# Kernel tuning notes

Measured on AMD Instinct MI355X. Metric: run time of the kernel, lower is better.

The kernel has to match this reference:

```python
import jax, jax.numpy as jnp
import numpy as np

N_NODES = 50000
N_EDGES = 800000
N_GRAPHS = 64
F_IN, H1, H2, H3, N_CLS = 128, 512, 256, 128, 10
BN_EPS = 1e-5


def setup_inputs() -> dict:
    key = jax.random.key(0)
    ks = jax.random.split(key, 16)

    def lin(k, fi, fo):
        return jax.random.normal(k, (fi, fo), jnp.float32) / np.sqrt(fi).astype(np.float32)

    return {
        "x": jax.random.normal(ks[0], (N_NODES, F_IN), jnp.float32),
        "edge_index": jax.random.randint(ks[1], (2, N_EDGES), 0, N_NODES),
        "batch": jnp.sort(jax.random.randint(ks[2], (N_NODES,), 0, N_GRAPHS)),
        "W1": lin(ks[3], F_IN, H1), "b1": jnp.zeros((H1,), jnp.float32),
        "g1": jnp.ones((H1,), jnp.float32), "be1": jnp.zeros((H1,), jnp.float32),
        "W2": lin(ks[4], H1, H2), "b2": jnp.zeros((H2,), jnp.float32),
        "g2": jnp.ones((H2,), jnp.float32), "be2": jnp.zeros((H2,), jnp.float32),
        "W3": lin(ks[5], H2, H3), "b3": jnp.zeros((H3,), jnp.float32),
        "g3": jnp.ones((H3,), jnp.float32), "be3": jnp.zeros((H3,), jnp.float32),
        "Wo": lin(ks[6], H3, N_CLS), "bo": jnp.zeros((N_CLS,), jnp.float32),
    }


def _gcn_conv(x, row, col, W, b):
    # PyG GCNConv: h = x @ W; add self-loops; sym-normalized scatter-add; + bias
    n = x.shape[0]
    h = x @ W
    loop = jnp.arange(n, dtype=row.dtype)
    row2 = jnp.concatenate([row, loop])  # source nodes
    col2 = jnp.concatenate([col, loop])  # target nodes
    deg = jax.ops.segment_sum(jnp.ones_like(col2, dtype=h.dtype), col2, num_segments=n)
    dinv = jnp.where(deg > 0, jax.lax.rsqrt(deg), 0.0)
    norm = (dinv[row2] * dinv[col2])[:, None]
    agg = jax.ops.segment_sum(h[row2] * norm, col2, num_segments=n)
    return agg + b


def _bn(x, g, b):
    # training-mode BatchNorm over node dim (biased variance, eps=1e-5)
    mean = jnp.mean(x, axis=0)
    var = jnp.mean(jnp.square(x - mean), axis=0)
    return g * (x - mean) * jax.lax.rsqrt(var + BN_EPS) + b


def reference(x, edge_index, batch, W1, b1, g1, be1, W2, b2, g2, be2,
              W3, b3, g3, be3, Wo, bo):
    row, col = edge_index[0], edge_index[1]
    h = jax.nn.relu(_bn(_gcn_conv(x, row, col, W1, b1), g1, be1))
    h = jax.nn.relu(_bn(_gcn_conv(h, row, col, W2, b2), g2, be2))
    h = jax.nn.relu(_bn(_gcn_conv(h, row, col, W3, b3), g3, be3))
    # global_mean_pool over graph ids
    sums = jax.ops.segment_sum(h, batch, num_segments=N_GRAPHS)
    cnt = jax.ops.segment_sum(jnp.ones((h.shape[0],), h.dtype), batch, num_segments=N_GRAPHS)
    pooled = sums / jnp.maximum(cnt, 1.0)[:, None]
    return pooled @ Wo + bo
```

## Files before the change

### kernel.cpp

```cpp
#include <hip/hip_runtime.h>
#include <hip/hip_bf16.h>
#include <cstdint>
#include <cstddef>

#define NNODES 50000
#define NGRAPHS 64

typedef short bf16x8 __attribute__((ext_vector_type(8)));
typedef float f32x4 __attribute__((ext_vector_type(4)));

__device__ inline float bf2f(unsigned short u) {
    return __uint_as_float(((unsigned)u) << 16);
}
__device__ inline unsigned short f2bf(float f) {
    unsigned u = __float_as_uint(f);
    return (unsigned short)((u + 0x7fff + ((u >> 16) & 1)) >> 16);
}
__device__ inline void unpack8(uint4 u, float* v) {
    v[0] = bf2f((unsigned short)(u.x & 0xffff)); v[1] = bf2f((unsigned short)(u.x >> 16));
    v[2] = bf2f((unsigned short)(u.y & 0xffff)); v[3] = bf2f((unsigned short)(u.y >> 16));
    v[4] = bf2f((unsigned short)(u.z & 0xffff)); v[5] = bf2f((unsigned short)(u.z >> 16));
    v[6] = bf2f((unsigned short)(u.w & 0xffff)); v[7] = bf2f((unsigned short)(u.w >> 16));
}

__global__ void deg_count_k(const int* __restrict__ col, int* __restrict__ cnt, int ne) {
    int i = blockIdx.x * blockDim.x + threadIdx.x;
    if (i < ne) atomicAdd(&cnt[col[i]], 1);
}

__global__ __launch_bounds__(256) void scan1_k(const int* __restrict__ cnt, int* __restrict__ offs,
                                               int* __restrict__ bsum, float* __restrict__ dinv, int n) {
    int t = threadIdx.x;
    int base = blockIdx.x * 1024 + t * 4;
    int4 v = {0, 0, 0, 0};
    if (base + 3 < n) v = *reinterpret_cast<const int4*>(cnt + base);
    else {
        if (base + 0 < n) v.x = cnt[base + 0];
        if (base + 1 < n) v.y = cnt[base + 1];
        if (base + 2 < n) v.z = cnt[base + 2];
    }
    if (base + 0 < n) dinv[base + 0] = rsqrtf((float)(v.x + 1));
    if (base + 1 < n) dinv[base + 1] = rsqrtf((float)(v.y + 1));
    if (base + 2 < n) dinv[base + 2] = rsqrtf((float)(v.z + 1));
    if (base + 3 < n) dinv[base + 3] = rsqrtf((float)(v.w + 1));

    int s = v.x + v.y + v.z + v.w;
    __shared__ int lds[256];
    lds[t] = s;
    __syncthreads();
    #pragma unroll
    for (int d = 1; d < 256; d <<= 1) {
        int u = (t >= d) ? lds[t - d] : 0;
        __syncthreads();
        lds[t] += u;
        __syncthreads();
    }
    int excl = lds[t] - s;
    if (t == 255) bsum[blockIdx.x] = lds[t];

    if (base + 3 < n) {
        int4 o;
        o.x = excl; o.y = excl + v.x; o.z = o.y + v.y; o.w = o.z + v.z;
        *reinterpret_cast<int4*>(offs + base) = o;
    } else {
        int e = excl;
        if (base + 0 < n) { offs[base + 0] = e; e += v.x; }
        if (base + 1 < n) { offs[base + 1] = e; e += v.y; }
        if (base + 2 < n) { offs[base + 2] = e; }
    }
}

__global__ __launch_bounds__(256) void scan2_k(int* __restrict__ bsum, int nb) {
    __shared__ int lds[256];
    int t = threadIdx.x;
    int v = (t < nb) ? bsum[t] : 0;
    lds[t] = v;
    __syncthreads();
    #pragma unroll
    for (int d = 1; d < 256; d <<= 1) {
        int u = (t >= d) ? lds[t - d] : 0;
        __syncthreads();
        lds[t] += u;
        __syncthreads();
    }
    if (t < nb) bsum[t] = lds[t] - v;
}

__global__ __launch_bounds__(256) void scan3_k(int* __restrict__ offs, const int* __restrict__ bsum, int n) {
    int base = blockIdx.x * 1024 + threadIdx.x * 4;
    int add = bsum[blockIdx.x];
    if (base + 3 < n) {
        int4 o = *reinterpret_cast<int4*>(offs + base);
        o.x += add; o.y += add; o.z += add; o.w += add;
        *reinterpret_cast<int4*>(offs + base) = o;
    } else {
        for (int k = 0; k < 4; ++k)
            if (base + k < n) offs[base + k] += add;
    }
}

__global__ void scatter_k(const int* __restrict__ row_, const int* __restrict__ col_,
                          const int* __restrict__ offs, int* __restrict__ fill,
                          int* __restrict__ csr_row, int ne) {
    int e = blockIdx.x * blockDim.x + threadIdx.x;
    if (e >= ne) return;
    int r = row_[e], c = col_[e];
    int pos = offs[c] + atomicAdd(&fill[c], 1);
    csr_row[pos] = r;
}

__global__ void cvt_scale_k(const float* __restrict__ in, const float* __restrict__ dinv,
                            unsigned short* __restrict__ out, int n) {
    long long i = (long long)blockIdx.x * blockDim.x + threadIdx.x;
    long long total4 = (long long)n * 32;
    if (i >= total4) return;
    int r = (int)(i >> 5);
    float d = dinv[r];
    float4 v = reinterpret_cast<const float4*>(in)[i];
    uint2 o;
    o.x = (unsigned)f2bf(v.x * d) | ((unsigned)f2bf(v.y * d) << 16);
    o.y = (unsigned)f2bf(v.z * d) | ((unsigned)f2bf(v.w * d) << 16);
    reinterpret_cast<uint2*>(out)[i] = o;
}

__global__ void wtrans_all_k(const float* __restrict__ W1, const float* __restrict__ W2,
                             const float* __restrict__ W3,
                             unsigned short* __restrict__ Wt1, unsigned short* __restrict__ Wt2,
                             unsigned short* __restrict__ Wt3) {
    int idx = blockIdx.x * blockDim.x + threadIdx.x;
    if (idx < 65536) {
        int k = idx >> 9, m = idx & 511;
        Wt1[m * 128 + k] = f2bf(W1[idx]);
    } else if (idx < 196608) {
        int j = idx - 65536;
        int k = j >> 8, m = j & 255;
        Wt2[m * 512 + k] = f2bf(W2[j]);
    } else if (idx < 229376) {
        int j = idx - 196608;
        int k = j >> 7, m = j & 127;
        Wt3[m * 256 + k] = f2bf(W3[j]);
    }
}

template<int FC>
__global__ void agg_s_k(const unsigned short* __restrict__ in, const int* __restrict__ offs,
                        const int* __restrict__ cnt, const int* __restrict__ csr_row,
                        const float* __restrict__ dinv, unsigned short* __restrict__ out, int n) {
    constexpr int F   = 64 * FC;
    constexpr int LPE = (FC == 4) ? 32 : 16;
    constexpr int EPL = 64 / LPE;
    int node = blockIdx.x * 4 + (threadIdx.x >> 6);
    if (node >= n) return;
    int lane = threadIdx.x & 63;
    int sub = lane / LPE;
    int fl  = lane % LPE;
    const size_t foff = (size_t)fl * 8;

    float acc[8] = {};
    if (sub == 0) {
        uint4 u = *reinterpret_cast<const uint4*>(in + (size_t)node * F + foff);
        float v[8]; unpack8(u, v);
        #pragma unroll
        for (int i = 0; i < 8; ++i) acc[i] = v[i];
    }

    int s = offs[node], e1 = s + cnt[node];
    int eb = s;
    for (; eb + 2 * EPL <= e1; eb += 2 * EPL) {
        int r0 = csr_row[eb + sub];
        int r1 = csr_row[eb + EPL + sub];
        uint4 u0 = *reinterpret_cast<const uint4*>(in + (size_t)r0 * F + foff);
        uint4 u1 = *reinterpret_cast<const uint4*>(in + (size_t)r1 * F + foff);
        float v0[8], v1[8];
        unpack8(u0, v0); unpack8(u1, v1);
        #pragma unroll
        for (int i = 0; i < 8; ++i) acc[i] += v0[i] + v1[i];
    }
    for (; eb < e1; eb += EPL) {
        int e = eb + sub;
        bool ok = e < e1;
        int r = csr_row[ok ? e : e1 - 1];
        uint4 u = *reinterpret_cast<const uint4*>(in + (size_t)r * F + foff);
        float v[8]; unpack8(u, v);
        if (ok) {
            #pragma unroll
            for (int i = 0; i < 8; ++i) acc[i] += v[i];
        }
    }

    #pragma unroll
    for (int d = LPE; d < 64; d <<= 1) {
        #pragma unroll
        for (int i = 0; i < 8; ++i) acc[i] += __shfl_xor(acc[i], d, 64);
    }

    if (sub == 0) {
        float dn = dinv[node];
        uint4 o;
        o.x = (unsigned)f2bf(acc[0] * dn) | ((unsigned)f2bf(acc[1] * dn) << 16);
        o.y = (unsigned)f2bf(acc[2] * dn) | ((unsigned)f2bf(acc[3] * dn) << 16);
        o.z = (unsigned)f2bf(acc[4] * dn) | ((unsigned)f2bf(acc[5] * dn) << 16);
        o.w = (unsigned)f2bf(acc[6] * dn) | ((unsigned)f2bf(acc[7] * dn) << 16);
        *reinterpret_cast<uint4*>(out + (size_t)node * F + foff) = o;
    }
}

template<bool BN_A, bool SCALE_OUT, bool STATS>
__global__ __launch_bounds__(256) void gemm_bt_k(const unsigned short* __restrict__ A,
                                                 const unsigned short* __restrict__ B,
                                                 unsigned short* __restrict__ C,
                                                 const float* __restrict__ scale,
                                                 const float* __restrict__ shift,
                                                 const float* __restrict__ dinv,
                                                 float* __restrict__ sums,
                                                 float* __restrict__ sqs,
                                                 int n, int K, int M) {
    __shared__ unsigned short As[128][40];
    __shared__ unsigned short Bs[128][40];
    int tid = threadIdx.x;
    int wid = tid >> 6, lane = tid & 63;
    int wr = wid >> 1, wc = wid & 1;
    int row0 = blockIdx.y * 128, col0 = blockIdx.x * 128;

    f32x4 acc[4][4] = {};

    for (int kt = 0; kt < K; kt += 32) {
        int c8 = (tid & 3) * 8;
        float4 sc0, sc1, sh0, sh1;
        if (BN_A) {
            sc0 = *reinterpret_cast<const float4*>(scale + kt + c8);
            sc1 = *reinterpret_cast<const float4*>(scale + kt + c8 + 4);
            sh0 = *reinterpret_cast<const float4*>(shift + kt + c8);
            sh1 = *reinterpret_cast<const float4*>(shift + kt + c8 + 4);
        }
        #pragma unroll
        for (int h = 0; h < 2; ++h) {
            int r = (tid >> 2) + h * 64;
            int gr = row0 + r;
            bf16x8 va = {};
            if (gr < n) va = *reinterpret_cast<const bf16x8*>(A + (size_t)gr * K + kt + c8);
            if (BN_A) {
                #pragma unroll
                for (int t = 0; t < 8; ++t) {
                    float sct = (t < 4) ? (&sc0.x)[t] : (&sc1.x)[t - 4];
                    float sht = (t < 4) ? (&sh0.x)[t] : (&sh1.x)[t - 4];
                    float f = bf2f((unsigned short)va[t]);
                    va[t] = (short)f2bf(fmaxf(f * sct + sht, 0.f));
                }
            }
            *reinterpret_cast<bf16x8*>(&As[r][c8]) = va;
            bf16x8 vb = *reinterpret_cast<const bf16x8*>(B + (size_t)(col0 + r) * K + kt + c8);
            *reinterpret_cast<bf16x8*>(&Bs[r][c8]) = vb;
        }
        __syncthreads();

        bf16x8 af[4], bfr[4];
        int koff = (lane >> 4) * 8;
        #pragma unroll
        for (int f = 0; f < 4; ++f) {
            af[f]  = *reinterpret_cast<const bf16x8*>(&As[wr * 64 + f * 16 + (lane & 15)][koff]);
            bfr[f] = *reinterpret_cast<const bf16x8*>(&Bs[wc * 64 + f * 16 + (lane & 15)][koff]);
        }
        #pragma unroll
        for (int i = 0; i < 4; ++i)
            #pragma unroll
            for (int j = 0; j < 4; ++j)
                acc[i][j] = __builtin_amdgcn_mfma_f32_16x16x32_bf16(af[i], bfr[j], acc[i][j], 0, 0, 0);
        __syncthreads();
    }

    #pragma unroll
    for (int i = 0; i < 4; ++i) {
        #pragma unroll
        for (int q = 0; q < 4; ++q) {
            int gr = row0 + wr * 64 + i * 16 + (lane >> 4) * 4 + q;
            if (gr < n) {
                float dr = SCALE_OUT ? dinv[gr] : 1.0f;
                #pragma unroll
                for (int j = 0; j < 4; ++j) {
                    int gc = col0 + wc * 64 + j * 16 + (lane & 15);
                    C[(size_t)gr * M + gc] = f2bf(acc[i][j][q] * dr);
                }
            }
        }
    }

    if (STATS) {
        #pragma unroll
        for (int j = 0; j < 4; ++j) {
            float s = 0.f, q = 0.f;
            #pragma unroll
            for (int i = 0; i < 4; ++i)
                #pragma unroll
                for (int p = 0; p < 4; ++p) {
                    float v = acc[i][j][p];
                    s += v; q += v * v;
                }
            s += __shfl_xor(s, 16, 64); s += __shfl_xor(s, 32, 64);
            q += __shfl_xor(q, 16, 64); q += __shfl_xor(q, 32, 64);
            if ((lane >> 4) == 0) {
                int gc = col0 + wc * 64 + j * 16 + (lane & 15);
                atomicAdd(&sums[gc], s);
                atomicAdd(&sqs[gc], q);
            }
        }
    }
}

template<int F>
__global__ __launch_bounds__(256) void bn_stats_k(const unsigned short* __restrict__ in,
                                                  float* __restrict__ stat, int n) {
    constexpr int G   = F / 8;
    constexpr int RPP = 256 / G;
    int g  = threadIdx.x & (G - 1);
    int rl = threadIdx.x / G;

    float s[8] = {}, q[8] = {};
    for (int r = blockIdx.x * RPP + rl; r < n; r += gridDim.x * RPP) {
        uint4 u = *reinterpret_cast<const uint4*>(in + (size_t)r * F + g * 8);
        float v[8]; unpack8(u, v);
        #pragma unroll
        for (int i = 0; i < 8; ++i) { s[i] += v[i]; q[i] += v[i] * v[i]; }
    }

    __shared__ float lds[RPP][F];
    #pragma unroll
    for (int i = 0; i < 8; ++i) lds[rl][g * 8 + i] = s[i];
    __syncthreads();
    if (threadIdx.x < F) {
        float t = 0.f;
        #pragma unroll
        for (int rr = 0; rr < RPP; ++rr) t += lds[rr][threadIdx.x];
        atomicAdd(&stat[threadIdx.x], t);
    }
    __syncthreads();
    #pragma unroll
    for (int i = 0; i < 8; ++i) lds[rl][g * 8 + i] = q[i];
    __syncthreads();
    if (threadIdx.x < F) {
        float t = 0.f;
        #pragma unroll
        for (int rr = 0; rr < RPP; ++rr) t += lds[rr][threadIdx.x];
        atomicAdd(&stat[F + threadIdx.x], t);
    }
}

__global__ void bn_finalize_k(const float* __restrict__ stat,
                              const float* __restrict__ g, const float* __restrict__ be,
                              float* __restrict__ scale, float* __restrict__ shift,
                              int F, float invn) {
    int f = blockIdx.x * blockDim.x + threadIdx.x;
    if (f >= F) return;
    float mean = stat[f] * invn;
    float var  = stat[F + f] * invn - mean * mean;
    float rstd = rsqrtf(var + 1e-5f);
    float sc = g[f] * rstd;
    scale[f] = sc;
    shift[f] = be[f] - mean * sc;
}

__global__ void bounds_k(const int* __restrict__ batch, int* __restrict__ start, int n) {
    int i = blockIdx.x * blockDim.x + threadIdx.x;
    if (i >= n) return;
    int b = batch[i];
    if (i == 0) {
        for (int g = 0; g <= b; ++g) start[g] = 0;
    } else {
        int pb = batch[i - 1];
        for (int g = pb + 1; g <= b; ++g) start[g] = i;
    }
    if (i == n - 1) {
        for (int g = b + 1; g <= NGRAPHS; ++g) start[g] = n;
    }
}

__global__ __launch_bounds__(256) void pool_part_k(const unsigned short* __restrict__ a,
                                                   const int* __restrict__ start,
                                                   const float* __restrict__ scale,
                                                   const float* __restrict__ shift,
                                                   float* __restrict__ partial) {
    int g = blockIdx.x, q = blockIdx.y;
    int s = start[g], e = start[g + 1];
    int nr = e - s;
    int c0 = s + (nr * q) / 4, c1 = s + (nr * (q + 1)) / 4;
    int tf = threadIdx.x & 15, tr = threadIdx.x >> 4;

    float sc[8], sh[8];
    #pragma unroll
    for (int i = 0; i < 8; ++i) { sc[i] = scale[tf * 8 + i]; sh[i] = shift[tf * 8 + i]; }

    float acc[8] = {};
    for (int r = c0 + tr; r < c1; r += 16) {
        uint4 u = *reinterpret_cast<const uint4*>(a + (size_t)r * 128 + tf * 8);
        float v[8]; unpack8(u, v);
        #pragma unroll
        for (int i = 0; i < 8; ++i) acc[i] += fmaxf(v[i] * sc[i] + sh[i], 0.f);
    }

    __shared__ float red[16][128];
    #pragma unroll
    for (int i = 0; i < 8; ++i) red[tr][tf * 8 + i] = acc[i];
    __syncthreads();
    int f = threadIdx.x;
    if (f < 128) {
        float s2 = 0.f;
        #pragma unroll
        for (int t = 0; t < 16; ++t) s2 += red[t][f];
        partial[((size_t)(g * 4 + q)) * 128 + f] = s2;
    }
}

__global__ void final_out_k(const float* __restrict__ partial, const int* __restrict__ start,
                            const float* __restrict__ Wo, const float* __restrict__ bo,
                            float* __restrict__ out) {
    int idx = blockIdx.x * blockDim.x + threadIdx.x;
    if (idx >= NGRAPHS * 10) return;
    int g = idx / 10, c = idx - g * 10;
    float cntf = (float)(start[g + 1] - start[g]);
    float inv = 1.0f / fmaxf(cntf, 1.0f);
    float s = bo[c];
    for (int k = 0; k < 128; ++k) {
        float pk = partial[(size_t)(g * 4 + 0) * 128 + k] + partial[(size_t)(g * 4 + 1) * 128 + k]
                 + partial[(size_t)(g * 4 + 2) * 128 + k] + partial[(size_t)(g * 4 + 3) * 128 + k];
        s += pk * inv * Wo[k * 10 + c];
    }
    out[idx] = s;
}

extern "C" void kernel_launch(void* const* d_in, const int* in_sizes, int n_in,
                              void* d_out, int out_size, void* d_ws, size_t ws_size,
                              hipStream_t stream) {
    const float* x   = (const float*)d_in[0];
    const int*   ei  = (const int*)d_in[1];
    const int*   bat = (const int*)d_in[2];
    const float* W1  = (const float*)d_in[3];
    const float* g1  = (const float*)d_in[5];
    const float* be1 = (const float*)d_in[6];
    const float* W2  = (const float*)d_in[7];
    const float* g2  = (const float*)d_in[9];
    const float* be2 = (const float*)d_in[10];
    const float* W3  = (const float*)d_in[11];
    const float* g3  = (const float*)d_in[13];
    const float* be3 = (const float*)d_in[14];
    const float* Wo  = (const float*)d_in[15];
    const float* bo  = (const float*)d_in[16];
    float* out = (float*)d_out;

    const int n  = in_sizes[2];
    const int ne = in_sizes[1] / 2;
    const int* row = ei;
    const int* col = ei + ne;
    const int NB = (n + 1023) / 1024;

    char* base = (char*)d_ws;
    size_t o = 0;
    auto alloc = [&](size_t bytes) -> char* {
        char* p = base + o;
        o += (bytes + 255) & ~(size_t)255;
        return p;
    };
    int*   cntfill = (int*)alloc((size_t)2 * n * 4);
    int*   cnt  = cntfill;
    int*   fill = cntfill + n;
    float* statall = (float*)alloc((size_t)3 * 1024 * 4);
    float* stat1 = statall;
    float* stat2 = statall + 1024;
    float* stat3 = statall + 2048;
    size_t zspan = (size_t)((char*)(statall + 3 * 1024) - (char*)cntfill);

    int*   offs  = (int*)alloc(n * 4);
    int*   bsum  = (int*)alloc(256 * 4);
    float* dinv  = (float*)alloc(n * 4);
    int*   start = (int*)alloc((NGRAPHS + 1) * 4);
    float* scale = (float*)alloc(512 * 4);
    float* shift = (float*)alloc(512 * 4);
    float* partial = (float*)alloc((size_t)NGRAPHS * 4 * 128 * 4);
    int*   csr_row = (int*)alloc((size_t)ne * 4);
    unsigned short* Wt1 = (unsigned short*)alloc((size_t)128 * 512 * 2);
    unsigned short* Wt2 = (unsigned short*)alloc((size_t)512 * 256 * 2);
    unsigned short* Wt3 = (unsigned short*)alloc((size_t)256 * 128 * 2);
    unsigned short* xs_bf  = (unsigned short*)alloc((size_t)n * 128 * 2);
    unsigned short* ax_bf  = (unsigned short*)alloc((size_t)n * 128 * 2);
    unsigned short* h1_bf  = (unsigned short*)alloc((size_t)n * 512 * 2);
    unsigned short* t2s_bf = (unsigned short*)alloc((size_t)n * 256 * 2);
    unsigned short* a2_bf  = (unsigned short*)alloc((size_t)n * 256 * 2);
    unsigned short* t3s_bf = (unsigned short*)alloc((size_t)n * 128 * 2);
    unsigned short* a3_bf  = (unsigned short*)alloc((size_t)n * 128 * 2);

    hipMemsetAsync(cntfill, 0, zspan, stream);
    deg_count_k<<<(ne + 255) / 256, 256, 0, stream>>>(col, cnt, ne);
    scan1_k<<<NB, 256, 0, stream>>>(cnt, offs, bsum, dinv, n);
    scan2_k<<<1, 256, 0, stream>>>(bsum, NB);
    scan3_k<<<NB, 256, 0, stream>>>(offs, bsum, n);
    scatter_k<<<(ne + 255) / 256, 256, 0, stream>>>(row, col, offs, fill, csr_row, ne);
    bounds_k<<<(n + 255) / 256, 256, 0, stream>>>(bat, start, n);

    cvt_scale_k<<<(unsigned)(((long long)n * 32 + 255) / 256), 256, 0, stream>>>(x, dinv, xs_bf, n);
    wtrans_all_k<<<896, 256, 0, stream>>>(W1, W2, W3, Wt1, Wt2, Wt3);

    agg_s_k<2><<<(n + 3) / 4, 256, 0, stream>>>(xs_bf, offs, cnt, csr_row, dinv, ax_bf, n);
    gemm_bt_k<false, false, true><<<dim3(4, (n + 127) / 128), 256, 0, stream>>>(
        ax_bf, Wt1, h1_bf, nullptr, nullptr, nullptr, stat1, stat1 + 512, n, 128, 512);
    bn_finalize_k<<<2, 256, 0, stream>>>(stat1, g1, be1, scale, shift, 512, 1.0f / n);

    gemm_bt_k<true, true, false><<<dim3(2, (n + 127) / 128), 256, 0, stream>>>(
        h1_bf, Wt2, t2s_bf, scale, shift, dinv, nullptr, nullptr, n, 512, 256);
    agg_s_k<4><<<(n + 3) / 4, 256, 0, stream>>>(t2s_bf, offs, cnt, csr_row, dinv, a2_bf, n);
    bn_stats_k<256><<<1024, 256, 0, stream>>>(a2_bf, stat2, n);
    bn_finalize_k<<<1, 256, 0, stream>>>(stat2, g2, be2, scale, shift, 256, 1.0f / n);

    gemm_bt_k<true, true, false><<<dim3(1, (n + 127) / 128), 256, 0, stream>>>(
        a2_bf, Wt3, t3s_bf, scale, shift, dinv, nullptr, nullptr, n, 256, 128);
    agg_s_k<2><<<(n + 3) / 4, 256, 0, stream>>>(t3s_bf, offs, cnt, csr_row, dinv, a3_bf, n);
    bn_stats_k<128><<<1024, 256, 0, stream>>>(a3_bf, stat3, n);
    bn_finalize_k<<<1, 256, 0, stream>>>(stat3, g3, be3, scale, shift, 128, 1.0f / n);

    pool_part_k<<<dim3(NGRAPHS, 4), 256, 0, stream>>>(a3_bf, start, scale, shift, partial);
    final_out_k<<<3, 256, 0, stream>>>(partial, start, Wo, bo, out);
}
```

Before: 506.2 us.

## Merge prep kernels and fold BN finalize into consumer kernels

Four independent preprocessing kernels (CSR scatter, graph bounds, input convert/scale, weight transpose) become one grid-stride kernel, and the three BN finalize kernels go away. Each consuming GEMM block, and the pool kernel, now computes the BN scale and shift from the raw statistics into shared memory. The aim is to cut launch overhead and serial gaps between small kernels. The cost is redundant per-block finalize work and extra shared memory in the GEMM, plus a serialized grid-stride prep kernel with mixed workloads.

```diff
diff --git a/kernel.cpp b/kernel.cpp
--- a/kernel.cpp
+++ b/kernel.cpp
@@ -3,7 +3,6 @@
 #include <cstdint>
 #include <cstddef>
 
-#define NNODES 50000
 #define NGRAPHS 64
 
 typedef short bf16x8 __attribute__((ext_vector_type(8)));
@@ -99,46 +98,56 @@
     }
 }
 
-__global__ void scatter_k(const int* __restrict__ row_, const int* __restrict__ col_,
-                          const int* __restrict__ offs, int* __restrict__ fill,
-                          int* __restrict__ csr_row, int ne) {
-    int e = blockIdx.x * blockDim.x + threadIdx.x;
-    if (e >= ne) return;
-    int r = row_[e], c = col_[e];
-    int pos = offs[c] + atomicAdd(&fill[c], 1);
-    csr_row[pos] = r;
-}
-
-__global__ void cvt_scale_k(const float* __restrict__ in, const float* __restrict__ dinv,
-                            unsigned short* __restrict__ out, int n) {
-    long long i = (long long)blockIdx.x * blockDim.x + threadIdx.x;
+__global__ void prep3_k(const int* __restrict__ row_, const int* __restrict__ col_,
+                        const int* __restrict__ offs, int* __restrict__ fill, int* __restrict__ csr_row,
+                        const int* __restrict__ bat, int* __restrict__ start,
+                        const float* __restrict__ x, const float* __restrict__ dinv,
+                        unsigned short* __restrict__ xs,
+                        const float* __restrict__ W1, const float* __restrict__ W2, const float* __restrict__ W3,
+                        unsigned short* __restrict__ Wt1, unsigned short* __restrict__ Wt2,
+                        unsigned short* __restrict__ Wt3, int n, int ne) {
+    int gsz  = gridDim.x * blockDim.x;
+    int gtid = blockIdx.x * blockDim.x + threadIdx.x;
+    for (int e = gtid; e < ne; e += gsz) {
+        int r = row_[e], c = col_[e];
+        int pos = offs[c] + atomicAdd(&fill[c], 1);
+        csr_row[pos] = r;
+    }
+    for (int i = gtid; i < n; i += gsz) {
+        int b = bat[i];
+        if (i == 0) {
+            for (int g = 0; g <= b; ++g) start[g] = 0;
+        } else {
+            int pb = bat[i - 1];
+            for (int g = pb + 1; g <= b; ++g) start[g] = i;
+        }
+        if (i == n - 1) {
+            for (int g = b + 1; g <= NGRAPHS; ++g) start[g] = n;
+        }
+    }
     long long total4 = (long long)n * 32;
-    if (i >= total4) return;
-    int r = (int)(i >> 5);
-    float d = dinv[r];
-    float4 v = reinterpret_cast<const float4*>(in)[i];
-    uint2 o;
-    o.x = (unsigned)f2bf(v.x * d) | ((unsigned)f2bf(v.y * d) << 16);
-    o.y = (unsigned)f2bf(v.z * d) | ((unsigned)f2bf(v.w * d) << 16);
-    reinterpret_cast<uint2*>(out)[i] = o;
-}
-
-__global__ void wtrans_all_k(const float* __restrict__ W1, const float* __restrict__ W2,
-                             const float* __restrict__ W3,
-                             unsigned short* __restrict__ Wt1, unsigned short* __restrict__ Wt2,
-                             unsigned short* __restrict__ Wt3) {
-    int idx = blockIdx.x * blockDim.x + threadIdx.x;
-    if (idx < 65536) {
-        int k = idx >> 9, m = idx & 511;
-        Wt1[m * 128 + k] = f2bf(W1[idx]);
-    } else if (idx < 196608) {
-        int j = idx - 65536;
-        int k = j >> 8, m = j & 255;
-        Wt2[m * 512 + k] = f2bf(W2[j]);
-    } else if (idx < 229376) {
-        int j = idx - 196608;
-        int k = j >> 7, m = j & 127;
-        Wt3[m * 256 + k] = f2bf(W3[j]);
+    for (long long i = gtid; i < total4; i += gsz) {
+        int r = (int)(i >> 5);
+        float d = dinv[r];
+        float4 v = reinterpret_cast<const float4*>(x)[i];
+        uint2 o;
+        o.x = (unsigned)f2bf(v.x * d) | ((unsigned)f2bf(v.y * d) << 16);
+        o.y = (unsigned)f2bf(v.z * d) | ((unsigned)f2bf(v.w * d) << 16);
+        reinterpret_cast<uint2*>(xs)[i] = o;
+    }
+    for (int idx = gtid; idx < 229376; idx += gsz) {
+        if (idx < 65536) {
+            int k = idx >> 9, m = idx & 511;
+            Wt1[m * 128 + k] = f2bf(W1[idx]);
+        } else if (idx < 196608) {
+            int j = idx - 65536;
+            int k = j >> 8, m = j & 255;
+            Wt2[m * 512 + k] = f2bf(W2[j]);
+        } else {
+            int j = idx - 196608;
+            int k = j >> 7, m = j & 127;
+            Wt3[m * 256 + k] = f2bf(W3[j]);
+        }
     }
 }
 
@@ -205,19 +214,35 @@
     }
 }
 
-template<bool BN_A, bool SCALE_OUT, bool STATS>
+template<bool BN_STAT, bool SCALE_OUT, bool STATS>
 __global__ __launch_bounds__(256) void gemm_bt_k(const unsigned short* __restrict__ A,
                                                  const unsigned short* __restrict__ B,
                                                  unsigned short* __restrict__ C,
-                                                 const float* __restrict__ scale,
-                                                 const float* __restrict__ shift,
+                                                 const float* __restrict__ stat_in,
+                                                 const float* __restrict__ gamma,
+                                                 const float* __restrict__ beta,
+                                                 float invn,
                                                  const float* __restrict__ dinv,
                                                  float* __restrict__ sums,
                                                  float* __restrict__ sqs,
                                                  int n, int K, int M) {
     __shared__ unsigned short As[128][40];
     __shared__ unsigned short Bs[128][40];
+    __shared__ float scs[BN_STAT ? 512 : 1];
+    __shared__ float shs[BN_STAT ? 512 : 1];
     int tid = threadIdx.x;
+
+    if (BN_STAT) {
+        for (int f = tid; f < K; f += 256) {
+            float mean = stat_in[f] * invn;
+            float var  = stat_in[K + f] * invn - mean * mean;
+            float sc = gamma[f] * rsqrtf(var + 1e-5f);
+            scs[f] = sc;
+            shs[f] = beta[f] - mean * sc;
+        }
+        __syncthreads();
+    }
+
     int wid = tid >> 6, lane = tid & 63;
     int wr = wid >> 1, wc = wid & 1;
     int row0 = blockIdx.y * 128, col0 = blockIdx.x * 128;
@@ -227,11 +252,11 @@
     for (int kt = 0; kt < K; kt += 32) {
         int c8 = (tid & 3) * 8;
         float4 sc0, sc1, sh0, sh1;
-        if (BN_A) {
-            sc0 = *reinterpret_cast<const float4*>(scale + kt + c8);
-            sc1 = *reinterpret_cast<const float4*>(scale + kt + c8 + 4);
-            sh0 = *reinterpret_cast<const float4*>(shift + kt + c8);
-            sh1 = *reinterpret_cast<const float4*>(shift + kt + c8 + 4);
+        if (BN_STAT) {
+            sc0 = *reinterpret_cast<const float4*>(&scs[kt + c8]);
+            sc1 = *reinterpret_cast<const float4*>(&scs[kt + c8 + 4]);
+            sh0 = *reinterpret_cast<const float4*>(&shs[kt + c8]);
+            sh1 = *reinterpret_cast<const float4*>(&shs[kt + c8 + 4]);
         }
         #pragma unroll
         for (int h = 0; h < 2; ++h) {
@@ -239,7 +264,7 @@
             int gr = row0 + r;
             bf16x8 va = {};
             if (gr < n) va = *reinterpret_cast<const bf16x8*>(A + (size_t)gr * K + kt + c8);
-            if (BN_A) {
+            if (BN_STAT) {
                 #pragma unroll
                 for (int t = 0; t < 8; ++t) {
                     float sct = (t < 4) ? (&sc0.x)[t] : (&sc1.x)[t - 4];
@@ -345,49 +370,34 @@
     }
 }
 
-__global__ void bn_finalize_k(const float* __restrict__ stat,
-                              const float* __restrict__ g, const float* __restrict__ be,
-                              float* __restrict__ scale, float* __restrict__ shift,
-                              int F, float invn) {
-    int f = blockIdx.x * blockDim.x + threadIdx.x;
-    if (f >= F) return;
-    float mean = stat[f] * invn;
-    float var  = stat[F + f] * invn - mean * mean;
-    float rstd = rsqrtf(var + 1e-5f);
-    float sc = g[f] * rstd;
-    scale[f] = sc;
-    shift[f] = be[f] - mean * sc;
-}
-
-__global__ void bounds_k(const int* __restrict__ batch, int* __restrict__ start, int n) {
-    int i = blockIdx.x * blockDim.x + threadIdx.x;
-    if (i >= n) return;
-    int b = batch[i];
-    if (i == 0) {
-        for (int g = 0; g <= b; ++g) start[g] = 0;
-    } else {
-        int pb = batch[i - 1];
-        for (int g = pb + 1; g <= b; ++g) start[g] = i;
-    }
-    if (i == n - 1) {
-        for (int g = b + 1; g <= NGRAPHS; ++g) start[g] = n;
-    }
-}
-
 __global__ __launch_bounds__(256) void pool_part_k(const unsigned short* __restrict__ a,
                                                    const int* __restrict__ start,
-                                                   const float* __restrict__ scale,
-                                                   const float* __restrict__ shift,
+                                                   const float* __restrict__ stat3,
+                                                   const float* __restrict__ g3,
+                                                   const float* __restrict__ be3,
+                                                   float invn,
                                                    float* __restrict__ partial) {
+    __shared__ float scp[128], shp[128];
+    __shared__ float red[16][128];
+    int tid = threadIdx.x;
+    if (tid < 128) {
+        float mean = stat3[tid] * invn;
+        float var  = stat3[128 + tid] * invn - mean * mean;
+        float sc = g3[tid] * rsqrtf(var + 1e-5f);
+        scp[tid] = sc;
+        shp[tid] = be3[tid] - mean * sc;
+    }
+    __syncthreads();
+
     int g = blockIdx.x, q = blockIdx.y;
     int s = start[g], e = start[g + 1];
     int nr = e - s;
     int c0 = s + (nr * q) / 4, c1 = s + (nr * (q + 1)) / 4;
-    int tf = threadIdx.x & 15, tr = threadIdx.x >> 4;
+    int tf = tid & 15, tr = tid >> 4;
 
     float sc[8], sh[8];
     #pragma unroll
-    for (int i = 0; i < 8; ++i) { sc[i] = scale[tf * 8 + i]; sh[i] = shift[tf * 8 + i]; }
+    for (int i = 0; i < 8; ++i) { sc[i] = scp[tf * 8 + i]; sh[i] = shp[tf * 8 + i]; }
 
     float acc[8] = {};
     for (int r = c0 + tr; r < c1; r += 16) {
@@ -397,16 +407,14 @@
         for (int i = 0; i < 8; ++i) acc[i] += fmaxf(v[i] * sc[i] + sh[i], 0.f);
     }
 
-    __shared__ float red[16][128];
     #pragma unroll
     for (int i = 0; i < 8; ++i) red[tr][tf * 8 + i] = acc[i];
     __syncthreads();
-    int f = threadIdx.x;
-    if (f < 128) {
+    if (tid < 128) {
         float s2 = 0.f;
         #pragma unroll
-        for (int t = 0; t < 16; ++t) s2 += red[t][f];
-        partial[((size_t)(g * 4 + q)) * 128 + f] = s2;
+        for (int t = 0; t < 16; ++t) s2 += red[t][tid];
+        partial[((size_t)(g * 4 + q)) * 128 + tid] = s2;
     }
 }
 
@@ -472,8 +480,6 @@
     int*   bsum  = (int*)alloc(256 * 4);
     float* dinv  = (float*)alloc(n * 4);
     int*   start = (int*)alloc((NGRAPHS + 1) * 4);
-    float* scale = (float*)alloc(512 * 4);
-    float* shift = (float*)alloc(512 * 4);
     float* partial = (float*)alloc((size_t)NGRAPHS * 4 * 128 * 4);
     int*   csr_row = (int*)alloc((size_t)ne * 4);
     unsigned short* Wt1 = (unsigned short*)alloc((size_t)128 * 512 * 2);
@@ -487,34 +493,30 @@
     unsigned short* t3s_bf = (unsigned short*)alloc((size_t)n * 128 * 2);
     unsigned short* a3_bf  = (unsigned short*)alloc((size_t)n * 128 * 2);
 
+    const float invn = 1.0f / (float)n;
+
     hipMemsetAsync(cntfill, 0, zspan, stream);
     deg_count_k<<<(ne + 255) / 256, 256, 0, stream>>>(col, cnt, ne);
     scan1_k<<<NB, 256, 0, stream>>>(cnt, offs, bsum, dinv, n);
     scan2_k<<<1, 256, 0, stream>>>(bsum, NB);
     scan3_k<<<NB, 256, 0, stream>>>(offs, bsum, n);
-    scatter_k<<<(ne + 255) / 256, 256, 0, stream>>>(row, col, offs, fill, csr_row, ne);
-    bounds_k<<<(n + 255) / 256, 256, 0, stream>>>(bat, start, n);
-
-    cvt_scale_k<<<(unsigned)(((long long)n * 32 + 255) / 256), 256, 0, stream>>>(x, dinv, xs_bf, n);
-    wtrans_all_k<<<896, 256, 0, stream>>>(W1, W2, W3, Wt1, Wt2, Wt3);
+    prep3_k<<<2048, 256, 0, stream>>>(row, col, offs, fill, csr_row, bat, start,
+                                      x, dinv, xs_bf, W1, W2, W3, Wt1, Wt2, Wt3, n, ne);
 
     agg_s_k<2><<<(n + 3) / 4, 256, 0, stream>>>(xs_bf, offs, cnt, csr_row, dinv, ax_bf, n);
     gemm_bt_k<false, false, true><<<dim3(4, (n + 127) / 128), 256, 0, stream>>>(
-        ax_bf, Wt1, h1_bf, nullptr, nullptr, nullptr, stat1, stat1 + 512, n, 128, 512);
-    bn_finalize_k<<<2, 256, 0, stream>>>(stat1, g1, be1, scale, shift, 512, 1.0f / n);
+        ax_bf, Wt1, h1_bf, nullptr, nullptr, nullptr, 0.f, nullptr, stat1, stat1 + 512, n, 128, 512);
 
     gemm_bt_k<true, true, false><<<dim3(2, (n + 127) / 128), 256, 0, stream>>>(
-        h1_bf, Wt2, t2s_bf, scale, shift, dinv, nullptr, nullptr, n, 512, 256);
+        h1_bf, Wt2, t2s_bf, stat1, g1, be1, invn, dinv, nullptr, nullptr, n, 512, 256);
     agg_s_k<4><<<(n + 3) / 4, 256, 0, stream>>>(t2s_bf, offs, cnt, csr_row, dinv, a2_bf, n);
     bn_stats_k<256><<<1024, 256, 0, stream>>>(a2_bf, stat2, n);
-    bn_finalize_k<<<1, 256, 0, stream>>>(stat2, g2, be2, scale, shift, 256, 1.0f / n);
 
     gemm_bt_k<true, true, false><<<dim3(1, (n + 127) / 128), 256, 0, stream>>>(
-        a2_bf, Wt3, t3s_bf, scale, shift, dinv, nullptr, nullptr, n, 256, 128);
+        a2_bf, Wt3, t3s_bf, stat2, g2, be2, invn, dinv, nullptr, nullptr, n, 256, 128);
     agg_s_k<2><<<(n + 3) / 4, 256, 0, stream>>>(t3s_bf, offs, cnt, csr_row, dinv, a3_bf, n);
     bn_stats_k<128><<<1024, 256, 0, stream>>>(a3_bf, stat3, n);
-    bn_finalize_k<<<1, 256, 0, stream>>>(stat3, g3, be3, scale, shift, 128, 1.0f / n);
-
-    pool_part_k<<<dim3(NGRAPHS, 4), 256, 0, stream>>>(a3_bf, start, scale, shift, partial);
+
+    pool_part_k<<<dim3(NGRAPHS, 4), 256, 0, stream>>>(a3_bf, start, stat3, g3, be3, invn, partial);
     final_out_k<<<3, 256, 0, stream>>>(partial, start, Wo, bo, out);
 }
```

Measured after the change: 491.0 us. 3.0% less time.
